# Optimization experiments

Measured on AMD Instinct MI355X. Metric: run time of the kernel, lower is better.

The kernel has to match this reference:

```python
import jax, jax.numpy as jnp
import numpy as np

TOKENS, D_IN, D_OUT = 8192, 2048, 8192

def setup_inputs() -> dict:
    key = jax.random.key(0)
    k1, k2, k3 = jax.random.split(key, 3)
    # kaiming_uniform-ish full-precision weights; exact init unimportant for math
    bound_w = float(np.sqrt(6.0 / D_IN))
    weight = jax.random.uniform(k1, (D_OUT, D_IN), jnp.float32, -bound_w, bound_w)
    bound_b = 1.0 / float(np.sqrt(D_IN))
    bias = jax.random.uniform(k2, (D_OUT,), jnp.float32, -bound_b, bound_b)
    inp = jax.random.normal(k3, (TOKENS, D_IN), jnp.float32)
    return {"input": inp, "weight": weight, "bias": bias}

def reference(input, weight, bias) -> jnp.ndarray:
    # BitNet-style: binarize weight to {-1,0,+1} via sign, scale by mean |W|
    scale = jnp.mean(jnp.abs(weight))            # scalar
    w_q = jnp.sign(weight) * scale               # [D_OUT, D_IN]
    # F.linear: input @ w_q.T + bias
    return jnp.einsum('ti,oi->to', input, w_q) + bias
```

## Files before the change

kernel.cpp:

```cpp
#include <hip/hip_runtime.h>

typedef unsigned short u16;
typedef short short8 __attribute__((ext_vector_type(8)));
typedef float floatx4 __attribute__((ext_vector_type(4)));

#define TOKENS 8192
#define DIN    2048
#define DOUT   8192
#define NELEM  (DOUT * DIN)


__device__ __forceinline__ u16 f2bf(float f) {
    unsigned u = __float_as_uint(f);
    unsigned r = (u + 0x7FFFu + ((u >> 16) & 1u)) >> 16;
    return (u16)r;
}

__device__ __forceinline__ void gld16(const void* src, void* lds) {
    __builtin_amdgcn_global_load_lds((__attribute__((address_space(1))) void*)src,
                                     (__attribute__((address_space(3))) void*)lds,
                                     16, 0, 0);
}


__global__ __launch_bounds__(256) void cvt_input_k(const float4* __restrict__ in,
                                                   ushort4* __restrict__ out, int n4) {
    int idx = blockIdx.x * 256 + threadIdx.x;
    int stride = gridDim.x * 256;
    for (int i = idx; i < n4; i += stride) {
        float4 v = in[i];
        ushort4 r;
        r.x = f2bf(v.x); r.y = f2bf(v.y); r.z = f2bf(v.z); r.w = f2bf(v.w);
        out[i] = r;
    }
}

__device__ __forceinline__ u16 sgnbf(float v) {
    return (v > 0.f) ? (u16)0x3F80 : ((v < 0.f) ? (u16)0xBF80 : (u16)0);
}

__global__ __launch_bounds__(256) void cvt_weight_k(const float4* __restrict__ w,
                                                    ushort4* __restrict__ out,
                                                    double* __restrict__ sacc, int n4) {
    int idx = blockIdx.x * 256 + threadIdx.x;
    int stride = gridDim.x * 256;
    float s = 0.f;
    for (int i = idx; i < n4; i += stride) {
        float4 v = w[i];
        ushort4 r;
        r.x = sgnbf(v.x); r.y = sgnbf(v.y); r.z = sgnbf(v.z); r.w = sgnbf(v.w);
        out[i] = r;
        s += fabsf(v.x) + fabsf(v.y) + fabsf(v.z) + fabsf(v.w);
    }
    for (int off = 32; off > 0; off >>= 1) s += __shfl_down(s, off);
    __shared__ float red[4];
    int lane = threadIdx.x & 63, wave = threadIdx.x >> 6;
    if (lane == 0) red[wave] = s;
    __syncthreads();
    if (threadIdx.x == 0)
        atomicAdd(sacc, (double)(red[0] + red[1] + red[2] + red[3]));
}


__global__ __launch_bounds__(256) void bitgemm_k(const u16* __restrict__ A,
                                                 const u16* __restrict__ B,
                                                 const float* __restrict__ bias,
                                                 const double* __restrict__ sacc,
                                                 float* __restrict__ C) {
    __shared__ __align__(16) u16 As[128 * 32];
    __shared__ __align__(16) u16 Bs[128 * 32];

    const int tid  = threadIdx.x;
    const int lane = tid & 63;
    const int wave = tid >> 6;
    const int m0 = blockIdx.y * 128;
    const int n0 = blockIdx.x * 128;
    const int wm = (wave >> 1) * 64;
    const int wn = (wave & 1) * 64;

    floatx4 acc[4][4];
    floatx4 z = {0.f, 0.f, 0.f, 0.f};
    for (int m = 0; m < 4; ++m)
        for (int n = 0; n < 4; ++n) acc[m][n] = z;

    const int c0 = tid,        r0 = c0 >> 2, kof0 = (c0 & 3) << 3;
    const int c1 = 256 + tid,  r1 = c1 >> 2, kof1 = (c1 & 3) << 3;

    const u16* a0 = A + (size_t)(m0 + r0) * DIN + kof0;
    const u16* a1 = A + (size_t)(m0 + r1) * DIN + kof1;
    const u16* b0 = B + (size_t)(n0 + r0) * DIN + kof0;
    const u16* b1 = B + (size_t)(n0 + r1) * DIN + kof1;

    u16* ldsA0 = As + (wave * 64) * 8;
    u16* ldsA1 = As + (256 + wave * 64) * 8;
    u16* ldsB0 = Bs + (wave * 64) * 8;
    u16* ldsB1 = Bs + (256 + wave * 64) * 8;

    const int frow = lane & 15;
    const int kgrp = (lane >> 4) * 8;
    const u16* aBase = As + (wm + frow) * 32 + kgrp;
    const u16* bBase = Bs + (wn + frow) * 32 + kgrp;

    for (int k0 = 0; k0 < DIN; k0 += 32) {
        gld16(a0 + k0, ldsA0);
        gld16(a1 + k0, ldsA1);
        gld16(b0 + k0, ldsB0);
        gld16(b1 + k0, ldsB1);
        __syncthreads();

        short8 af[4], bf[4];
        for (int m = 0; m < 4; ++m) af[m] = *(const short8*)(aBase + m * 16 * 32);
        for (int n = 0; n < 4; ++n) bf[n] = *(const short8*)(bBase + n * 16 * 32);
        for (int m = 0; m < 4; ++m)
            for (int n = 0; n < 4; ++n)
                acc[m][n] = __builtin_amdgcn_mfma_f32_16x16x32_bf16(af[m], bf[n], acc[m][n], 0, 0, 0);
        __syncthreads();
    }

    const float scale = (float)(sacc[0] * (1.0 / (double)NELEM));
    const int rowb = (lane >> 4) * 4;
    const int colb = lane & 15;
    for (int n = 0; n < 4; ++n) {
        const int o = n0 + wn + n * 16 + colb;
        const float bo = bias[o];
        for (int m = 0; m < 4; ++m) {
            const int t = m0 + wm + m * 16 + rowb;
            floatx4 v = acc[m][n];
            for (int r = 0; r < 4; ++r)
                C[(size_t)(t + r) * DOUT + o] = v[r] * scale + bo;
        }
    }
}


extern "C" void kernel_launch(void* const* d_in, const int* in_sizes, int n_in,
                              void* d_out, int out_size, void* d_ws, size_t ws_size,
                              hipStream_t stream) {
    const float* inp  = (const float*)d_in[0];
    const float* wgt  = (const float*)d_in[1];
    const float* bias = (const float*)d_in[2];
    float* out = (float*)d_out;

    u16* Abf = (u16*)d_ws;
    u16* Bbf = Abf + NELEM;
    double* sacc = (double*)(Bbf + NELEM);

    hipMemsetAsync(sacc, 0, sizeof(double), stream);
    cvt_weight_k<<<2048, 256, 0, stream>>>((const float4*)wgt, (ushort4*)Bbf, sacc, NELEM / 4);
    cvt_input_k<<<2048, 256, 0, stream>>>((const float4*)inp, (ushort4*)Abf, NELEM / 4);

    dim3 grid(DOUT / 128, TOKENS / 128);
    bitgemm_k<<<grid, 256, 0, stream>>>(Abf, Bbf, bias, sacc, out);
}
```

Measured before the change: 652.0 us.

## Rewrite bit-GEMM with 256x256 tiles, triple-buffered LDS, swizzle, and deterministic scale reduce

```diff
diff --git a/kernel.cpp b/kernel.cpp
--- a/kernel.cpp
+++ b/kernel.cpp
@@ -9,6 +9,12 @@
 #define DOUT   8192
 #define NELEM  (DOUT * DIN)
 
+#define BM 256
+#define BN 256
+#define BK 32
+#define NT (DIN / BK)
+#define NBUF 3
+
 
 __device__ __forceinline__ u16 f2bf(float f) {
     unsigned u = __float_as_uint(f);
@@ -16,9 +22,9 @@
     return (u16)r;
 }
 
-__device__ __forceinline__ void gld16(const void* src, void* lds) {
+__device__ __forceinline__ void gld16(const void* src, void* ldsp) {
     __builtin_amdgcn_global_load_lds((__attribute__((address_space(1))) void*)src,
-                                     (__attribute__((address_space(3))) void*)lds,
+                                     (__attribute__((address_space(3))) void*)ldsp,
                                      16, 0, 0);
 }
 
@@ -41,7 +47,7 @@
 
 __global__ __launch_bounds__(256) void cvt_weight_k(const float4* __restrict__ w,
                                                     ushort4* __restrict__ out,
-                                                    double* __restrict__ sacc, int n4) {
+                                                    float* __restrict__ part, int n4) {
     int idx = blockIdx.x * 256 + threadIdx.x;
     int stride = gridDim.x * 256;
     float s = 0.f;
@@ -57,77 +63,128 @@
     int lane = threadIdx.x & 63, wave = threadIdx.x >> 6;
     if (lane == 0) red[wave] = s;
     __syncthreads();
+    if (threadIdx.x == 0) part[blockIdx.x] = red[0] + red[1] + red[2] + red[3];
+}
+
+__global__ __launch_bounds__(256) void reduce_scale_k(const float* __restrict__ part,
+                                                      float* __restrict__ scalep, int n) {
+    double s = 0.0;
+    for (int i = threadIdx.x; i < n; i += 256) s += (double)part[i];
+    for (int off = 32; off > 0; off >>= 1) s += __shfl_down(s, off);
+    __shared__ double red[4];
+    int lane = threadIdx.x & 63, wave = threadIdx.x >> 6;
+    if (lane == 0) red[wave] = s;
+    __syncthreads();
     if (threadIdx.x == 0)
-        atomicAdd(sacc, (double)(red[0] + red[1] + red[2] + red[3]));
-}
-
-
-__global__ __launch_bounds__(256) void bitgemm_k(const u16* __restrict__ A,
-                                                 const u16* __restrict__ B,
-                                                 const float* __restrict__ bias,
-                                                 const double* __restrict__ sacc,
-                                                 float* __restrict__ C) {
-    __shared__ __align__(16) u16 As[128 * 32];
-    __shared__ __align__(16) u16 Bs[128 * 32];
+        scalep[0] = (float)((red[0] + red[1] + red[2] + red[3]) / (double)NELEM);
+}
+
+
+__global__ __launch_bounds__(512, 2) void bitgemm_k(const u16* __restrict__ A,
+                                                    const u16* __restrict__ B,
+                                                    const float* __restrict__ bias,
+                                                    const float* __restrict__ scalep,
+                                                    float* __restrict__ C) {
+    __shared__ __align__(16) char lds[NBUF * 32768];
 
     const int tid  = threadIdx.x;
     const int lane = tid & 63;
     const int wave = tid >> 6;
-    const int m0 = blockIdx.y * 128;
-    const int n0 = blockIdx.x * 128;
-    const int wm = (wave >> 1) * 64;
-    const int wn = (wave & 1) * 64;
-
-    floatx4 acc[4][4];
+
+    const int flat = blockIdx.y * gridDim.x + blockIdx.x;
+    const int cpx  = (gridDim.x * gridDim.y) >> 3;
+    const int swz  = (flat & 7) * cpx + (flat >> 3);
+    const int m0 = (swz >> 5) * BM;
+    const int n0 = (swz & 31) * BN;
+
+    const int wm = (wave >> 2) * 128;
+    const int wn = (wave & 3) * 64;
+
+    const u16* srcA[2];
+    const u16* srcB[2];
+#pragma unroll
+    for (int c = 0; c < 2; ++c) {
+        int lin = c * 8192 + tid * 16;
+        int p   = lin >> 7;
+        int sp  = (lin >> 4) & 7;
+        int s   = sp ^ (p & 7);
+        int row = 2 * p + (s >> 2);
+        int g   = s & 3;
+        srcA[c] = A + (size_t)(m0 + row) * DIN + g * 8;
+        srcB[c] = B + (size_t)(n0 + row) * DIN + g * 8;
+    }
+
+#define STAGE(kt, sb) do {                                                   \
+        char* base_ = lds + (sb) * 32768;                                    \
+        gld16(srcA[0] + (kt) * BK, base_ +         wave * 1024);             \
+        gld16(srcA[1] + (kt) * BK, base_ +  8192 + wave * 1024);             \
+        gld16(srcB[0] + (kt) * BK, base_ + 16384 + wave * 1024);             \
+        gld16(srcB[1] + (kt) * BK, base_ + 24576 + wave * 1024);             \
+    } while (0)
+
+    const int gg = lane >> 4;
+    const int rA = wm + (lane & 15);
+    const int pA = rA >> 1;
+    const int offA = pA * 128 + ((((rA & 1) << 2) | gg) ^ (pA & 7)) * 16;
+    const int rB = wn + (lane & 15);
+    const int pB = rB >> 1;
+    const int offB = 16384 + pB * 128 + ((((rB & 1) << 2) | gg) ^ (pB & 7)) * 16;
+
+    floatx4 acc[8][4];
     floatx4 z = {0.f, 0.f, 0.f, 0.f};
-    for (int m = 0; m < 4; ++m)
+#pragma unroll
+    for (int m = 0; m < 8; ++m)
+#pragma unroll
         for (int n = 0; n < 4; ++n) acc[m][n] = z;
 
-    const int c0 = tid,        r0 = c0 >> 2, kof0 = (c0 & 3) << 3;
-    const int c1 = 256 + tid,  r1 = c1 >> 2, kof1 = (c1 & 3) << 3;
-
-    const u16* a0 = A + (size_t)(m0 + r0) * DIN + kof0;
-    const u16* a1 = A + (size_t)(m0 + r1) * DIN + kof1;
-    const u16* b0 = B + (size_t)(n0 + r0) * DIN + kof0;
-    const u16* b1 = B + (size_t)(n0 + r1) * DIN + kof1;
-
-    u16* ldsA0 = As + (wave * 64) * 8;
-    u16* ldsA1 = As + (256 + wave * 64) * 8;
-    u16* ldsB0 = Bs + (wave * 64) * 8;
-    u16* ldsB1 = Bs + (256 + wave * 64) * 8;
-
-    const int frow = lane & 15;
-    const int kgrp = (lane >> 4) * 8;
-    const u16* aBase = As + (wm + frow) * 32 + kgrp;
-    const u16* bBase = Bs + (wn + frow) * 32 + kgrp;
-
-    for (int k0 = 0; k0 < DIN; k0 += 32) {
-        gld16(a0 + k0, ldsA0);
-        gld16(a1 + k0, ldsA1);
-        gld16(b0 + k0, ldsB0);
-        gld16(b1 + k0, ldsB1);
-        __syncthreads();
-
-        short8 af[4], bf[4];
-        for (int m = 0; m < 4; ++m) af[m] = *(const short8*)(aBase + m * 16 * 32);
-        for (int n = 0; n < 4; ++n) bf[n] = *(const short8*)(bBase + n * 16 * 32);
-        for (int m = 0; m < 4; ++m)
+    STAGE(0, 0);
+    STAGE(1, 1);
+    asm volatile("s_waitcnt vmcnt(4)" ::: "memory");
+    __builtin_amdgcn_s_barrier();
+    __builtin_amdgcn_sched_barrier(0);
+
+    for (int t = 0; t < NT; ++t) {
+        if (t + 2 < NT) STAGE(t + 2, (t + 2) % 3);
+
+        const char* bufA = lds + (t % 3) * 32768 + offA;
+        const char* bufB = lds + (t % 3) * 32768 + offB;
+        short8 af[8], bq[4];
+#pragma unroll
+        for (int m = 0; m < 8; ++m) af[m] = *(const short8*)(bufA + m * 1024);
+#pragma unroll
+        for (int n = 0; n < 4; ++n) bq[n] = *(const short8*)(bufB + n * 1024);
+
+        __builtin_amdgcn_s_setprio(1);
+#pragma unroll
+        for (int m = 0; m < 8; ++m)
+#pragma unroll
             for (int n = 0; n < 4; ++n)
-                acc[m][n] = __builtin_amdgcn_mfma_f32_16x16x32_bf16(af[m], bf[n], acc[m][n], 0, 0, 0);
-        __syncthreads();
-    }
-
-    const float scale = (float)(sacc[0] * (1.0 / (double)NELEM));
-    const int rowb = (lane >> 4) * 4;
-    const int colb = lane & 15;
+                acc[m][n] = __builtin_amdgcn_mfma_f32_16x16x32_bf16(af[m], bq[n], acc[m][n], 0, 0, 0);
+        __builtin_amdgcn_s_setprio(0);
+
+        if (t + 1 < NT) {
+            if (t + 2 < NT) asm volatile("s_waitcnt vmcnt(4)" ::: "memory");
+            else            asm volatile("s_waitcnt vmcnt(0)" ::: "memory");
+            __builtin_amdgcn_s_barrier();
+            __builtin_amdgcn_sched_barrier(0);
+        }
+    }
+#undef STAGE
+
+    const float scale = scalep[0];
+    const int rowe = (lane >> 4) * 4;
+    const int cole = lane & 15;
+#pragma unroll
     for (int n = 0; n < 4; ++n) {
-        const int o = n0 + wn + n * 16 + colb;
+        const int o = n0 + wn + n * 16 + cole;
         const float bo = bias[o];
-        for (int m = 0; m < 4; ++m) {
-            const int t = m0 + wm + m * 16 + rowb;
+#pragma unroll
+        for (int m = 0; m < 8; ++m) {
+            const int trow = m0 + wm + m * 16 + rowe;
             floatx4 v = acc[m][n];
+#pragma unroll
             for (int r = 0; r < 4; ++r)
-                C[(size_t)(t + r) * DOUT + o] = v[r] * scale + bo;
+                C[(size_t)(trow + r) * DOUT + o] = v[r] * scale + bo;
         }
     }
 }
@@ -143,12 +200,13 @@
 
     u16* Abf = (u16*)d_ws;
     u16* Bbf = Abf + NELEM;
-    double* sacc = (double*)(Bbf + NELEM);
-
-    hipMemsetAsync(sacc, 0, sizeof(double), stream);
-    cvt_weight_k<<<2048, 256, 0, stream>>>((const float4*)wgt, (ushort4*)Bbf, sacc, NELEM / 4);
-    cvt_input_k<<<2048, 256, 0, stream>>>((const float4*)inp, (ushort4*)Abf, NELEM / 4);
-
-    dim3 grid(DOUT / 128, TOKENS / 128);
-    bitgemm_k<<<grid, 256, 0, stream>>>(Abf, Bbf, bias, sacc, out);
-}
+    float* part   = (float*)(Bbf + NELEM);
+    float* scalep = part + 1024;
+
+    cvt_weight_k<<<1024, 256, 0, stream>>>((const float4*)wgt, (ushort4*)Bbf, part, NELEM / 4);
+    cvt_input_k<<<1024, 256, 0, stream>>>((const float4*)inp, (ushort4*)Abf, NELEM / 4);
+    reduce_scale_k<<<1, 256, 0, stream>>>(part, scalep, 1024);
+
+    dim3 grid(DOUT / BN, TOKENS / BM);
+    bitgemm_k<<<grid, 512, 0, stream>>>(Abf, Bbf, bias, scalep, out);
+}
```

New measurement: 597.5 us. 1.09x faster.
